# Kernel optimization log

Measured on AMD Instinct MI355X. Metric: run time of the kernel, lower is better.

## Reference

```python
import jax, jax.numpy as jnp
import numpy as np

N_NODES = 100000
N_EDGES = 1600000
IN_F = 32
HID = 128


def setup_inputs() -> dict:
    key = jax.random.key(0)
    ks = jax.random.split(key, 8)
    x = jax.random.normal(ks[0], (N_NODES, IN_F), dtype=jnp.float32)
    edge_index = jax.random.randint(ks[1], (2, N_EDGES), 0, N_NODES, dtype=jnp.int64)
    # Glorot-ish scaled weights
    W1 = jax.random.normal(ks[2], (IN_F, HID), dtype=jnp.float32) / np.sqrt(IN_F)
    b1 = jnp.zeros((HID,), dtype=jnp.float32)
    W2 = jax.random.normal(ks[3], (HID, HID), dtype=jnp.float32) / np.sqrt(HID)
    b2 = jnp.zeros((HID,), dtype=jnp.float32)
    W3 = jax.random.normal(ks[4], (HID, IN_F), dtype=jnp.float32) / np.sqrt(HID)
    b3 = jnp.zeros((IN_F,), dtype=jnp.float32)
    return {"x": x, "edge_index": edge_index, "W1": W1, "b1": b1,
            "W2": W2, "b2": b2, "W3": W3, "b3": b3}


def _gcn_norm(edge_index, n_nodes):
    # Add self-loops (PyG GCNConv default) and compute symmetric normalization
    loops = jnp.arange(n_nodes, dtype=edge_index.dtype)
    src = jnp.concatenate([edge_index[0], loops])
    dst = jnp.concatenate([edge_index[1], loops])
    ones = jnp.ones(src.shape[0], dtype=jnp.float32)
    deg = jax.ops.segment_sum(ones, dst, num_segments=n_nodes)
    deg_inv_sqrt = jnp.where(deg > 0, jax.lax.rsqrt(deg), 0.0)
    norm = deg_inv_sqrt[src] * deg_inv_sqrt[dst]  # [E + N]
    return src, dst, norm


def _gcn_conv(x, src, dst, norm, W, b, n_nodes):
    h = x @ W                                # [N, out] transform first (smaller msgs when out<in)
    msg = h[src] * norm[:, None]             # gather + edge-wise scale  [E+N, out]
    out = jax.ops.segment_sum(msg, dst, num_segments=n_nodes)  # scatter-add
    return out + b


def reference(x, edge_index, W1, b1, W2, b2, W3, b3):
    n = x.shape[0]
    src, dst, norm = _gcn_norm(edge_index, n)
    h = jax.nn.relu(_gcn_conv(x, src, dst, norm, W1, b1, n))
    h = jax.nn.relu(_gcn_conv(h, src, dst, norm, W2, b2, n))
    h = jax.nn.relu(_gcn_conv(h, src, dst, norm, W3, b3, n))
    return h
```

## Files before the change

kernel.cpp:

```cpp
#include <hip/hip_runtime.h>
#include <hip/hip_fp16.h>

#define N_NODES 100000
#define N_EDGES 1600000
#define IN_F 32
#define HID 128
#define BSHIFT 9
#define BSIZE 512
#define NBUCK 196
#define EPB 4096
#define NBB 391
#define REC_STRIDE 9728
#define COL_STRIDE 17408

typedef _Float16 half8 __attribute__((ext_vector_type(8)));
typedef float floatx4 __attribute__((ext_vector_type(4)));

__global__ __launch_bounds__(256) void k_wprep(const float* __restrict__ W1,
                                               const float* __restrict__ W2,
                                               const float* __restrict__ W3,
                                               _Float16* __restrict__ Wt) {
    const int bid = blockIdx.x, t = threadIdx.x;
    if (bid < 64) {
        int idx = bid * 256 + t;
        int n = idx >> 7, k = idx & 127;
        Wt[4096 + idx] = (_Float16)W2[k * HID + n];
    } else if (bid < 80) {
        int idx = (bid - 64) * 256 + t;
        int n = idx >> 5, k = idx & 31;
        Wt[n * 32 + k] = (_Float16)W1[k * HID + n];
    } else {
        int idx = (bid - 80) * 256 + t;
        int n = idx >> 7, k = idx & 127;
        Wt[20480 + idx] = (_Float16)W3[k * IN_F + n];
    }
}


__global__ __launch_bounds__(256) void k_bucket(const int* __restrict__ src,
                                                const int* __restrict__ dst,
                                                int* __restrict__ bcur,
                                                unsigned* __restrict__ rec) {
    __shared__ int hist[256];
    __shared__ int lbase[256];
    const int e0 = blockIdx.x * EPB;
    hist[threadIdx.x] = 0;
    __syncthreads();

    unsigned rk[16]; short bk[16];
#pragma unroll
    for (int k = 0; k < 16; ++k) {
        int e = e0 + k * 256 + threadIdx.x;
        if (e < N_EDGES) {
            int d = dst[e];
            int b = d >> BSHIFT;
            bk[k] = (short)b;
            rk[k] = ((unsigned)src[e] << BSHIFT) | (unsigned)(d & (BSIZE - 1));
            atomicAdd(&hist[b], 1);
        } else bk[k] = -1;
    }
    __syncthreads();
    int c = hist[threadIdx.x];
    lbase[threadIdx.x] =
        (c > 0) ? threadIdx.x * REC_STRIDE + atomicAdd(&bcur[threadIdx.x], c) : 0;
    __syncthreads();
    hist[threadIdx.x] = 0;
    __syncthreads();
#pragma unroll
    for (int k = 0; k < 16; ++k) {
        if (bk[k] >= 0) {
            int off = atomicAdd(&hist[bk[k]], 1);
            rec[lbase[bk[k]] + off] = rk[k];
        }
    }
}

__global__ __launch_bounds__(256) void k_fill3p(const unsigned* __restrict__ rec,
                                                const int* __restrict__ bcur,
                                                const float2* __restrict__ x2,
                                                int* __restrict__ ideg,
                                                int* __restrict__ cursor,
                                                int* __restrict__ col,
                                                __half2* __restrict__ t1) {
    __shared__ int lcnt[BSIZE];
    __shared__ int lcur[BSIZE];
    __shared__ int lend[BSIZE];
    __shared__ int s[256];
    const int b = blockIdx.x;
    const int t = threadIdx.x;
    const int n0 = b << BSHIFT;
    const int rbeg = b * REC_STRIDE;
    const int rend = rbeg + bcur[b];
    const int pbeg = b * COL_STRIDE;

    lcnt[t] = 0;
    lcnt[t + 256] = 0;
    __syncthreads();
    for (int i = rbeg + t; i < rend; i += 256)
        atomicAdd(&lcnt[rec[i] & (BSIZE - 1)], 1);
    __syncthreads();

    int a0 = lcnt[2 * t], a1 = lcnt[2 * t + 1];
    int p0 = (a0 + 15) & ~15, p1 = (a1 + 15) & ~15;
    int pv = p0 + p1;
    s[t] = pv;
    __syncthreads();
    for (int off = 1; off < 256; off <<= 1) {
        int v = (t >= off) ? s[t - off] : 0;
        __syncthreads();
        s[t] += v;
        __syncthreads();
    }
    int ex = s[t] - pv;
    int c0 = pbeg + ex;
    int c1 = c0 + p0;
    lcur[2 * t]     = c0;  lend[2 * t]     = c0 + p0;
    lcur[2 * t + 1] = c1;  lend[2 * t + 1] = c1 + p1;
    __syncthreads();

    for (int i = t; i < BSIZE; i += 256) {
        int n = n0 + i;
        if (n < N_NODES) {
            ideg[n]   = lcnt[i];
            cursor[n] = lcur[i];
        }
    }
    __syncthreads();
    for (int i = rbeg + t; i < rend; i += 256) {
        unsigned r = rec[i];
        int slot = atomicAdd(&lcur[r & (BSIZE - 1)], 1);
        col[slot] = (int)(r >> BSHIFT);
    }
    __syncthreads();
    for (int i = t; i < BSIZE; i += 256) {
        int e2 = lend[i];
        for (int k = lcur[i]; k < e2; ++k) col[k] = N_NODES;
    }

    if (b == 0 && t < 16) ((unsigned*)t1)[N_NODES * 16 + t] = 0u;
    for (int idx = t; idx < BSIZE * 16; idx += 256) {
        int loc = idx >> 4, j = idx & 15;
        int n = n0 + loc;
        if (n < N_NODES) {
            float dis = rsqrtf(1.0f + (float)lcnt[loc]);
            float2 v = x2[(size_t)n * 16 + j];
            t1[(size_t)n * 16 + j] = __floats2half2_rn(v.x * dis, v.y * dis);
        }
    }
}


__global__ __launch_bounds__(256) void k_gather32_pre(
    const int* __restrict__ cursor, const int* __restrict__ ideg,
    const int* __restrict__ col, const _Float16* __restrict__ T,
    _Float16* __restrict__ OUT) {
    const int lane = threadIdx.x & 63;
    const int slot = lane >> 2;
    const int fl   = lane & 3;
    const int wid  = blockIdx.x * 4 + (threadIdx.x >> 6);
    const int wstride = gridDim.x * 4;

    for (int node = wid; node < N_NODES; node += wstride) {
        int begin = cursor[node];
        int d     = ideg[node];
        int nb    = (d + 15) >> 4;
        float acc[8];
        if (slot == 0) {
            half8 v = *(const half8*)(T + (size_t)node * IN_F + fl * 8);
#pragma unroll
            for (int i = 0; i < 8; ++i) acc[i] = (float)v[i];
        } else {
#pragma unroll
            for (int i = 0; i < 8; ++i) acc[i] = 0.f;
        }
        const int* cp = col + begin + slot;
        int itb = 0;
        for (; itb + 2 <= nb; itb += 2, cp += 32) {
            int s0 = cp[0];
            int s1 = cp[16];
            half8 v0 = *(const half8*)(T + (size_t)s0 * IN_F + fl * 8);
            half8 v1 = *(const half8*)(T + (size_t)s1 * IN_F + fl * 8);
#pragma unroll
            for (int i = 0; i < 8; ++i) acc[i] += (float)v0[i] + (float)v1[i];
        }
        if (itb < nb) {
            int s0 = cp[0];
            half8 v0 = *(const half8*)(T + (size_t)s0 * IN_F + fl * 8);
#pragma unroll
            for (int i = 0; i < 8; ++i) acc[i] += (float)v0[i];
        }
#pragma unroll
        for (int m = 4; m < 64; m <<= 1)
#pragma unroll
            for (int i = 0; i < 8; ++i) acc[i] += __shfl_xor(acc[i], m, 64);
        if (slot == 0) {
            float dis = rsqrtf(1.0f + (float)d);
            half8 o;
#pragma unroll
            for (int i = 0; i < 8; ++i) o[i] = (_Float16)(acc[i] * dis);
            *(half8*)(OUT + (size_t)node * IN_F + fl * 8) = o;
        }
    }
}

__global__ __launch_bounds__(256) void k_gather32_fin(
    const int* __restrict__ cursor, const int* __restrict__ ideg,
    const int* __restrict__ col, const _Float16* __restrict__ T,
    const float* __restrict__ b, float* __restrict__ OUT) {
    const int lane = threadIdx.x & 63;
    const int slot = lane >> 2;
    const int fl   = lane & 3;
    const int wid  = blockIdx.x * 4 + (threadIdx.x >> 6);
    const int wstride = gridDim.x * 4;

    float4 bb0 = *(const float4*)(b + fl * 8);
    float4 bb1 = *(const float4*)(b + fl * 8 + 4);
    float bias[8] = {bb0.x, bb0.y, bb0.z, bb0.w, bb1.x, bb1.y, bb1.z, bb1.w};

    for (int node = wid; node < N_NODES; node += wstride) {
        int begin = cursor[node];
        int d     = ideg[node];
        int nb    = (d + 15) >> 4;
        float acc[8];
        if (slot == 0) {
            half8 v = *(const half8*)(T + (size_t)node * IN_F + fl * 8);
#pragma unroll
            for (int i = 0; i < 8; ++i) acc[i] = (float)v[i];
        } else {
#pragma unroll
            for (int i = 0; i < 8; ++i) acc[i] = 0.f;
        }
        const int* cp = col + begin + slot;
        int itb = 0;
        for (; itb + 2 <= nb; itb += 2, cp += 32) {
            int s0 = cp[0];
            int s1 = cp[16];
            half8 v0 = *(const half8*)(T + (size_t)s0 * IN_F + fl * 8);
            half8 v1 = *(const half8*)(T + (size_t)s1 * IN_F + fl * 8);
#pragma unroll
            for (int i = 0; i < 8; ++i) acc[i] += (float)v0[i] + (float)v1[i];
        }
        if (itb < nb) {
            int s0 = cp[0];
            half8 v0 = *(const half8*)(T + (size_t)s0 * IN_F + fl * 8);
#pragma unroll
            for (int i = 0; i < 8; ++i) acc[i] += (float)v0[i];
        }
#pragma unroll
        for (int m = 4; m < 64; m <<= 1)
#pragma unroll
            for (int i = 0; i < 8; ++i) acc[i] += __shfl_xor(acc[i], m, 64);
        if (slot == 0) {
            float dis = rsqrtf(1.0f + (float)d);
            float o[8];
#pragma unroll
            for (int i = 0; i < 8; ++i) {
                float v = acc[i] * dis + bias[i];
                o[i] = v > 0.f ? v : 0.f;
            }
            float* op = OUT + (size_t)node * IN_F + fl * 8;
            *(float4*)op       = make_float4(o[0], o[1], o[2], o[3]);
            *(float4*)(op + 4) = make_float4(o[4], o[5], o[6], o[7]);
        }
    }
}


__global__ __launch_bounds__(256, 4) void k_xform12(
    const _Float16* __restrict__ z, const _Float16* __restrict__ W1t,
    const float* __restrict__ b1, const _Float16* __restrict__ W2t,
    const int* __restrict__ ideg, _Float16* __restrict__ T) {
    if (blockIdx.x == 0 && threadIdx.x < 64)
        ((unsigned*)(T + (size_t)N_NODES * HID))[threadIdx.x] = 0u;
    __shared__ _Float16 H1s[64 * 136];

    const int lane = threadIdx.x & 63;
    const int wave = threadIdx.x >> 6;
    const int m16 = lane & 15, quad = lane >> 4;
    const int row0 = blockIdx.x * 64 + wave * 16;
    if (row0 >= N_NODES) return;

    {
        int arow = row0 + m16; if (arow >= N_NODES) arow = N_NODES - 1;
        half8 a = *(const half8*)(z + (size_t)arow * IN_F + quad * 8);
        floatx4 acc[8];
#pragma unroll
        for (int t = 0; t < 8; ++t) acc[t] = (floatx4){0.f, 0.f, 0.f, 0.f};
#pragma unroll
        for (int t = 0; t < 8; ++t) {
            half8 bf = *(const half8*)(W1t + (t * 16 + m16) * 32 + quad * 8);
            acc[t] = __builtin_amdgcn_mfma_f32_16x16x32_f16(a, bf, acc[t], 0, 0, 0);
        }
#pragma unroll
        for (int t = 0; t < 8; ++t) {
            int c = t * 16 + m16;
            float bj = b1[c];
#pragma unroll
            for (int r = 0; r < 4; ++r) {
                float v = acc[t][r] + bj;
                H1s[((wave * 16 + quad * 4 + r) * 136) + c] =
                    (_Float16)(v > 0.f ? v : 0.f);
            }
        }
    }
    __syncthreads();

    const _Float16* hp = &H1s[(wave * 16 + m16) * 136 + quad * 8];
    half8 a[4];
#pragma unroll
    for (int kk = 0; kk < 4; ++kk) a[kk] = *(const half8*)(hp + kk * 32);

    floatx4 acc[8];
#pragma unroll
    for (int t = 0; t < 8; ++t) acc[t] = (floatx4){0.f, 0.f, 0.f, 0.f};
#pragma unroll
    for (int t = 0; t < 8; ++t) {
        const _Float16* wp = W2t + (t * 16 + m16) * 128 + quad * 8;
#pragma unroll
        for (int kk = 0; kk < 4; ++kk) {
            half8 bf = *(const half8*)(wp + kk * 32);
            acc[t] = __builtin_amdgcn_mfma_f32_16x16x32_f16(a[kk], bf, acc[t], 0, 0, 0);
        }
    }
    float dis[4];
#pragma unroll
    for (int r = 0; r < 4; ++r) {
        int row = row0 + quad * 4 + r;
        dis[r] = (row < N_NODES) ? rsqrtf(1.0f + (float)ideg[row]) : 0.f;
    }
#pragma unroll
    for (int t = 0; t < 8; ++t) {
        int c = t * 16 + m16;
#pragma unroll
        for (int r = 0; r < 4; ++r) {
            int row = row0 + quad * 4 + r;
            if (row < N_NODES)
                T[(size_t)row * HID + c] = (_Float16)(acc[t][r] * dis[r]);
        }
    }
}

__global__ __launch_bounds__(256, 4) void k_g128x3(
    const int* __restrict__ cursor, const int* __restrict__ ideg,
    const int* __restrict__ col, const _Float16* __restrict__ T,
    const float* __restrict__ b2, const _Float16* __restrict__ W3t,
    _Float16* __restrict__ T3) {
    if (blockIdx.x == 0 && threadIdx.x < 16)
        ((unsigned*)(T3 + (size_t)N_NODES * IN_F))[threadIdx.x] = 0u;
    __shared__ _Float16 H2s[64 * 136];

    const int lane = threadIdx.x & 63;
    const int wave = threadIdx.x >> 6;
    const int slot = lane >> 4;
    const int fl   = lane & 15;
    const int row0 = blockIdx.x * 64;

    float4 bb0 = *(const float4*)(b2 + fl * 8);
    float4 bb1 = *(const float4*)(b2 + fl * 8 + 4);
    float bias[8] = {bb0.x, bb0.y, bb0.z, bb0.w, bb1.x, bb1.y, bb1.z, bb1.w};

    for (int k = 0; k < 16; ++k) {
        int node = row0 + wave * 16 + k;
        if (node >= N_NODES) break;
        int begin = cursor[node];
        int d     = ideg[node];
        int nb    = (d + 15) >> 4;
        float acc[8];
        if (slot == 0) {
            half8 v = *(const half8*)(T + (size_t)node * HID + fl * 8);
#pragma unroll
            for (int i = 0; i < 8; ++i) acc[i] = (float)v[i];
        } else {
#pragma unroll
            for (int i = 0; i < 8; ++i) acc[i] = 0.f;
        }
        const int* cp = col + begin + slot * 4;
        for (int itb = 0; itb < nb; ++itb, cp += 16) {
            int4 cc = *(const int4*)cp;
            half8 v0 = *(const half8*)(T + (size_t)cc.x * HID + fl * 8);
            half8 v1 = *(const half8*)(T + (size_t)cc.y * HID + fl * 8);
            half8 v2 = *(const half8*)(T + (size_t)cc.z * HID + fl * 8);
            half8 v3 = *(const half8*)(T + (size_t)cc.w * HID + fl * 8);
#pragma unroll
            for (int i = 0; i < 8; ++i)
                acc[i] += ((float)v0[i] + (float)v1[i]) + ((float)v2[i] + (float)v3[i]);
        }
#pragma unroll
        for (int m = 16; m < 64; m <<= 1)
#pragma unroll
            for (int i = 0; i < 8; ++i) acc[i] += __shfl_xor(acc[i], m, 64);
        if (slot == 0) {
            float dis = rsqrtf(1.0f + (float)d);
            half8 o;
#pragma unroll
            for (int i = 0; i < 8; ++i) {
                float v = acc[i] * dis + bias[i];
                o[i] = (_Float16)(v > 0.f ? v : 0.f);
            }
            *(half8*)&H2s[(wave * 16 + k) * 136 + fl * 8] = o;
        }
    }
    __syncthreads();

    const _Float16* hp = &H2s[(wave * 16 + fl) * 136 + slot * 8];
    half8 a[4];
#pragma unroll
    for (int kk = 0; kk < 4; ++kk) a[kk] = *(const half8*)(hp + kk * 32);

    floatx4 acc3[2];
#pragma unroll
    for (int t = 0; t < 2; ++t) acc3[t] = (floatx4){0.f, 0.f, 0.f, 0.f};
#pragma unroll
    for (int t = 0; t < 2; ++t) {
        const _Float16* wp = W3t + (t * 16 + fl) * 128 + slot * 8;
#pragma unroll
        for (int kk = 0; kk < 4; ++kk) {
            half8 bf = *(const half8*)(wp + kk * 32);
            acc3[t] = __builtin_amdgcn_mfma_f32_16x16x32_f16(a[kk], bf, acc3[t], 0, 0, 0);
        }
    }
    float dis[4];
#pragma unroll
    for (int r = 0; r < 4; ++r) {
        int row = row0 + wave * 16 + slot * 4 + r;
        dis[r] = (row < N_NODES) ? rsqrtf(1.0f + (float)ideg[row]) : 0.f;
    }
#pragma unroll
    for (int t = 0; t < 2; ++t) {
        int c = t * 16 + fl;
#pragma unroll
        for (int r = 0; r < 4; ++r) {
            int row = row0 + wave * 16 + slot * 4 + r;
            if (row < N_NODES)
                T3[(size_t)row * IN_F + c] = (_Float16)(acc3[t][r] * dis[r]);
        }
    }
}


extern "C" void kernel_launch(void* const* d_in, const int* in_sizes, int n_in,
                              void* d_out, int out_size, void* d_ws, size_t ws_size,
                              hipStream_t stream) {
    const float* x  = (const float*)d_in[0];
    const int*   ei = (const int*)d_in[1];
    const float* W1 = (const float*)d_in[2];
    const float* b1 = (const float*)d_in[3];
    const float* W2 = (const float*)d_in[4];
    const float* b2 = (const float*)d_in[5];
    const float* W3 = (const float*)d_in[6];
    const float* b3 = (const float*)d_in[7];
    float* out = (float*)d_out;

    const int* src = ei;
    const int* dst = ei + N_EDGES;

    int*      ideg   = (int*)d_ws;
    int*      cursor = ideg + 102400;
    int*      bcur   = cursor + 102400;
    int*      col    = bcur + 256;
    unsigned* rec    = (unsigned*)(col + NBUCK * COL_STRIDE);
    _Float16* Wt     = (_Float16*)(rec + NBUCK * REC_STRIDE);
    _Float16* t1h    = Wt + 24576;
    _Float16* z      = t1h + 3200064;
    _Float16* T2h    = z + 3200064;
    _Float16* T3h    = T2h + 12800128;

    const int xgrid = (N_NODES + 63) / 64;

    hipMemsetAsync(bcur, 0, 256 * sizeof(int), stream);
    k_wprep<<<96, 256, 0, stream>>>(W1, W2, W3, Wt);

    k_bucket<<<NBB, 256, 0, stream>>>(src, dst, bcur, rec);
    k_fill3p<<<NBUCK, 256, 0, stream>>>(rec, bcur, (const float2*)x,
                                        ideg, cursor, col, (__half2*)t1h);

    k_gather32_pre<<<2048, 256, 0, stream>>>(cursor, ideg, col, t1h, z);
    k_xform12<<<xgrid, 256, 0, stream>>>(z, Wt, b1, Wt + 4096, ideg, T2h);

    k_g128x3<<<xgrid, 256, 0, stream>>>(cursor, ideg, col, T2h, b2,
                                        Wt + 20480, T3h);

    k_gather32_fin<<<2048, 256, 0, stream>>>(cursor, ideg, col, T3h, b3, out);
}
```

Baseline: 323.9 us.

## Split 32-wide feature tables into two 16-wide planes for cache-friendlier gathers

The 32-feature fp16 node tables (t1, z, T3) are stored as two separate 16-column planes. The 32-wide gather kernels now make two passes, one per plane, with 32 edge slots per wave instead of 16. The idea is that each pass touches a table half the size, so more of it stays resident in L2/LLC during random neighbour gathers. Column padding per node grows to a multiple of 32 to match the wider slot count. The trade-offs are reading the column index lists twice, more padding work, and a larger col buffer; the 128-wide gather loop count is adjusted to the new padding.

```diff
diff --git a/kernel.cpp b/kernel.cpp
--- a/kernel.cpp
+++ b/kernel.cpp
@@ -11,7 +11,8 @@
 #define EPB 4096
 #define NBB 391
 #define REC_STRIDE 9728
-#define COL_STRIDE 17408
+#define COL_STRIDE 25600
+#define ZSL 1600016
 
 typedef _Float16 half8 __attribute__((ext_vector_type(8)));
 typedef float floatx4 __attribute__((ext_vector_type(4)));
@@ -81,7 +82,7 @@
                                                 int* __restrict__ ideg,
                                                 int* __restrict__ cursor,
                                                 int* __restrict__ col,
-                                                __half2* __restrict__ t1) {
+                                                _Float16* __restrict__ t1) {
     __shared__ int lcnt[BSIZE];
     __shared__ int lcur[BSIZE];
     __shared__ int lend[BSIZE];
@@ -101,7 +102,7 @@
     __syncthreads();
 
     int a0 = lcnt[2 * t], a1 = lcnt[2 * t + 1];
-    int p0 = (a0 + 15) & ~15, p1 = (a1 + 15) & ~15;
+    int p0 = (a0 + 31) & ~31, p1 = (a1 + 31) & ~31;
     int pv = p0 + p1;
     s[t] = pv;
     __syncthreads();
@@ -137,14 +138,19 @@
         for (int k = lcur[i]; k < e2; ++k) col[k] = N_NODES;
     }
 
-    if (b == 0 && t < 16) ((unsigned*)t1)[N_NODES * 16 + t] = 0u;
+    if (b == 0 && t < 16) {
+        if (t < 8) ((unsigned*)(t1 + (size_t)N_NODES * 16))[t] = 0u;
+        else       ((unsigned*)(t1 + ZSL + (size_t)N_NODES * 16))[t - 8] = 0u;
+    }
     for (int idx = t; idx < BSIZE * 16; idx += 256) {
         int loc = idx >> 4, j = idx & 15;
         int n = n0 + loc;
         if (n < N_NODES) {
             float dis = rsqrtf(1.0f + (float)lcnt[loc]);
             float2 v = x2[(size_t)n * 16 + j];
-            t1[(size_t)n * 16 + j] = __floats2half2_rn(v.x * dis, v.y * dis);
+            int p = j >> 3, jj = j & 7;
+            *(__half2*)(t1 + (size_t)p * ZSL + (size_t)n * 16 + jj * 2) =
+                __floats2half2_rn(v.x * dis, v.y * dis);
         }
     }
 }
@@ -155,50 +161,54 @@
     const int* __restrict__ col, const _Float16* __restrict__ T,
     _Float16* __restrict__ OUT) {
     const int lane = threadIdx.x & 63;
-    const int slot = lane >> 2;
-    const int fl   = lane & 3;
+    const int slot = lane >> 1;
+    const int fl   = lane & 1;
     const int wid  = blockIdx.x * 4 + (threadIdx.x >> 6);
     const int wstride = gridDim.x * 4;
 
-    for (int node = wid; node < N_NODES; node += wstride) {
-        int begin = cursor[node];
-        int d     = ideg[node];
-        int nb    = (d + 15) >> 4;
-        float acc[8];
-        if (slot == 0) {
-            half8 v = *(const half8*)(T + (size_t)node * IN_F + fl * 8);
-#pragma unroll
-            for (int i = 0; i < 8; ++i) acc[i] = (float)v[i];
-        } else {
-#pragma unroll
-            for (int i = 0; i < 8; ++i) acc[i] = 0.f;
-        }
-        const int* cp = col + begin + slot;
-        int itb = 0;
-        for (; itb + 2 <= nb; itb += 2, cp += 32) {
-            int s0 = cp[0];
-            int s1 = cp[16];
-            half8 v0 = *(const half8*)(T + (size_t)s0 * IN_F + fl * 8);
-            half8 v1 = *(const half8*)(T + (size_t)s1 * IN_F + fl * 8);
-#pragma unroll
-            for (int i = 0; i < 8; ++i) acc[i] += (float)v0[i] + (float)v1[i];
-        }
-        if (itb < nb) {
-            int s0 = cp[0];
-            half8 v0 = *(const half8*)(T + (size_t)s0 * IN_F + fl * 8);
-#pragma unroll
-            for (int i = 0; i < 8; ++i) acc[i] += (float)v0[i];
-        }
-#pragma unroll
-        for (int m = 4; m < 64; m <<= 1)
-#pragma unroll
-            for (int i = 0; i < 8; ++i) acc[i] += __shfl_xor(acc[i], m, 64);
-        if (slot == 0) {
-            float dis = rsqrtf(1.0f + (float)d);
-            half8 o;
-#pragma unroll
-            for (int i = 0; i < 8; ++i) o[i] = (_Float16)(acc[i] * dis);
-            *(half8*)(OUT + (size_t)node * IN_F + fl * 8) = o;
+    for (int p = 0; p < 2; ++p) {
+        const _Float16* Tp = T + (size_t)p * ZSL;
+        _Float16* Op = OUT + (size_t)p * ZSL;
+        for (int node = wid; node < N_NODES; node += wstride) {
+            int begin = cursor[node];
+            int d     = ideg[node];
+            int nb    = (d + 31) >> 5;
+            float acc[8];
+            if (slot == 0) {
+                half8 v = *(const half8*)(Tp + (size_t)node * 16 + fl * 8);
+#pragma unroll
+                for (int i = 0; i < 8; ++i) acc[i] = (float)v[i];
+            } else {
+#pragma unroll
+                for (int i = 0; i < 8; ++i) acc[i] = 0.f;
+            }
+            const int* cp = col + begin + slot;
+            int itb = 0;
+            for (; itb + 2 <= nb; itb += 2, cp += 64) {
+                int s0 = cp[0];
+                int s1 = cp[32];
+                half8 v0 = *(const half8*)(Tp + (size_t)s0 * 16 + fl * 8);
+                half8 v1 = *(const half8*)(Tp + (size_t)s1 * 16 + fl * 8);
+#pragma unroll
+                for (int i = 0; i < 8; ++i) acc[i] += (float)v0[i] + (float)v1[i];
+            }
+            if (itb < nb) {
+                int s0 = cp[0];
+                half8 v0 = *(const half8*)(Tp + (size_t)s0 * 16 + fl * 8);
+#pragma unroll
+                for (int i = 0; i < 8; ++i) acc[i] += (float)v0[i];
+            }
+#pragma unroll
+            for (int m = 2; m < 64; m <<= 1)
+#pragma unroll
+                for (int i = 0; i < 8; ++i) acc[i] += __shfl_xor(acc[i], m, 64);
+            if (slot == 0) {
+                float dis = rsqrtf(1.0f + (float)d);
+                half8 o;
+#pragma unroll
+                for (int i = 0; i < 8; ++i) o[i] = (_Float16)(acc[i] * dis);
+                *(half8*)(Op + (size_t)node * 16 + fl * 8) = o;
+            }
         }
     }
 }
@@ -208,59 +218,61 @@
     const int* __restrict__ col, const _Float16* __restrict__ T,
     const float* __restrict__ b, float* __restrict__ OUT) {
     const int lane = threadIdx.x & 63;
-    const int slot = lane >> 2;
-    const int fl   = lane & 3;
+    const int slot = lane >> 1;
+    const int fl   = lane & 1;
     const int wid  = blockIdx.x * 4 + (threadIdx.x >> 6);
     const int wstride = gridDim.x * 4;
 
-    float4 bb0 = *(const float4*)(b + fl * 8);
-    float4 bb1 = *(const float4*)(b + fl * 8 + 4);
-    float bias[8] = {bb0.x, bb0.y, bb0.z, bb0.w, bb1.x, bb1.y, bb1.z, bb1.w};
-
-    for (int node = wid; node < N_NODES; node += wstride) {
-        int begin = cursor[node];
-        int d     = ideg[node];
-        int nb    = (d + 15) >> 4;
-        float acc[8];
-        if (slot == 0) {
-            half8 v = *(const half8*)(T + (size_t)node * IN_F + fl * 8);
-#pragma unroll
-            for (int i = 0; i < 8; ++i) acc[i] = (float)v[i];
-        } else {
-#pragma unroll
-            for (int i = 0; i < 8; ++i) acc[i] = 0.f;
-        }
-        const int* cp = col + begin + slot;
-        int itb = 0;
-        for (; itb + 2 <= nb; itb += 2, cp += 32) {
-            int s0 = cp[0];
-            int s1 = cp[16];
-            half8 v0 = *(const half8*)(T + (size_t)s0 * IN_F + fl * 8);
-            half8 v1 = *(const half8*)(T + (size_t)s1 * IN_F + fl * 8);
-#pragma unroll
-            for (int i = 0; i < 8; ++i) acc[i] += (float)v0[i] + (float)v1[i];
-        }
-        if (itb < nb) {
-            int s0 = cp[0];
-            half8 v0 = *(const half8*)(T + (size_t)s0 * IN_F + fl * 8);
-#pragma unroll
-            for (int i = 0; i < 8; ++i) acc[i] += (float)v0[i];
-        }
-#pragma unroll
-        for (int m = 4; m < 64; m <<= 1)
-#pragma unroll
-            for (int i = 0; i < 8; ++i) acc[i] += __shfl_xor(acc[i], m, 64);
-        if (slot == 0) {
-            float dis = rsqrtf(1.0f + (float)d);
-            float o[8];
-#pragma unroll
-            for (int i = 0; i < 8; ++i) {
-                float v = acc[i] * dis + bias[i];
-                o[i] = v > 0.f ? v : 0.f;
-            }
-            float* op = OUT + (size_t)node * IN_F + fl * 8;
-            *(float4*)op       = make_float4(o[0], o[1], o[2], o[3]);
-            *(float4*)(op + 4) = make_float4(o[4], o[5], o[6], o[7]);
+    for (int p = 0; p < 2; ++p) {
+        const _Float16* Tp = T + (size_t)p * ZSL;
+        float4 bb0 = *(const float4*)(b + p * 16 + fl * 8);
+        float4 bb1 = *(const float4*)(b + p * 16 + fl * 8 + 4);
+        float bias[8] = {bb0.x, bb0.y, bb0.z, bb0.w, bb1.x, bb1.y, bb1.z, bb1.w};
+        for (int node = wid; node < N_NODES; node += wstride) {
+            int begin = cursor[node];
+            int d     = ideg[node];
+            int nb    = (d + 31) >> 5;
+            float acc[8];
+            if (slot == 0) {
+                half8 v = *(const half8*)(Tp + (size_t)node * 16 + fl * 8);
+#pragma unroll
+                for (int i = 0; i < 8; ++i) acc[i] = (float)v[i];
+            } else {
+#pragma unroll
+                for (int i = 0; i < 8; ++i) acc[i] = 0.f;
+            }
+            const int* cp = col + begin + slot;
+            int itb = 0;
+            for (; itb + 2 <= nb; itb += 2, cp += 64) {
+                int s0 = cp[0];
+                int s1 = cp[32];
+                half8 v0 = *(const half8*)(Tp + (size_t)s0 * 16 + fl * 8);
+                half8 v1 = *(const half8*)(Tp + (size_t)s1 * 16 + fl * 8);
+#pragma unroll
+                for (int i = 0; i < 8; ++i) acc[i] += (float)v0[i] + (float)v1[i];
+            }
+            if (itb < nb) {
+                int s0 = cp[0];
+                half8 v0 = *(const half8*)(Tp + (size_t)s0 * 16 + fl * 8);
+#pragma unroll
+                for (int i = 0; i < 8; ++i) acc[i] += (float)v0[i];
+            }
+#pragma unroll
+            for (int m = 2; m < 64; m <<= 1)
+#pragma unroll
+                for (int i = 0; i < 8; ++i) acc[i] += __shfl_xor(acc[i], m, 64);
+            if (slot == 0) {
+                float dis = rsqrtf(1.0f + (float)d);
+                float o[8];
+#pragma unroll
+                for (int i = 0; i < 8; ++i) {
+                    float v = acc[i] * dis + bias[i];
+                    o[i] = v > 0.f ? v : 0.f;
+                }
+                float* op = OUT + (size_t)node * IN_F + p * 16 + fl * 8;
+                *(float4*)op       = make_float4(o[0], o[1], o[2], o[3]);
+                *(float4*)(op + 4) = make_float4(o[4], o[5], o[6], o[7]);
+            }
         }
     }
 }
@@ -282,7 +294,8 @@
 
     {
         int arow = row0 + m16; if (arow >= N_NODES) arow = N_NODES - 1;
-        half8 a = *(const half8*)(z + (size_t)arow * IN_F + quad * 8);
+        half8 a = *(const half8*)(z + (size_t)(quad >> 1) * ZSL +
+                                  (size_t)arow * 16 + (quad & 1) * 8);
         floatx4 acc[8];
 #pragma unroll
         for (int t = 0; t < 8; ++t) acc[t] = (floatx4){0.f, 0.f, 0.f, 0.f};
@@ -345,8 +358,11 @@
     const int* __restrict__ col, const _Float16* __restrict__ T,
     const float* __restrict__ b2, const _Float16* __restrict__ W3t,
     _Float16* __restrict__ T3) {
-    if (blockIdx.x == 0 && threadIdx.x < 16)
-        ((unsigned*)(T3 + (size_t)N_NODES * IN_F))[threadIdx.x] = 0u;
+    if (blockIdx.x == 0 && threadIdx.x < 16) {
+        int t = threadIdx.x;
+        if (t < 8) ((unsigned*)(T3 + (size_t)N_NODES * 16))[t] = 0u;
+        else       ((unsigned*)(T3 + ZSL + (size_t)N_NODES * 16))[t - 8] = 0u;
+    }
     __shared__ _Float16 H2s[64 * 136];
 
     const int lane = threadIdx.x & 63;
@@ -364,7 +380,7 @@
         if (node >= N_NODES) break;
         int begin = cursor[node];
         int d     = ideg[node];
-        int nb    = (d + 15) >> 4;
+        int nb    = ((d + 31) & ~31) >> 4;
         float acc[8];
         if (slot == 0) {
             half8 v = *(const half8*)(T + (size_t)node * HID + fl * 8);
@@ -427,12 +443,12 @@
     }
 #pragma unroll
     for (int t = 0; t < 2; ++t) {
-        int c = t * 16 + fl;
 #pragma unroll
         for (int r = 0; r < 4; ++r) {
             int row = row0 + wave * 16 + slot * 4 + r;
             if (row < N_NODES)
-                T3[(size_t)row * IN_F + c] = (_Float16)(acc3[t][r] * dis[r]);
+                T3[(size_t)t * ZSL + (size_t)row * 16 + fl] =
+                    (_Float16)(acc3[t][r] * dis[r]);
         }
     }
 }
@@ -461,8 +477,8 @@
     unsigned* rec    = (unsigned*)(col + NBUCK * COL_STRIDE);
     _Float16* Wt     = (_Float16*)(rec + NBUCK * REC_STRIDE);
     _Float16* t1h    = Wt + 24576;
-    _Float16* z      = t1h + 3200064;
-    _Float16* T2h    = z + 3200064;
+    _Float16* z      = t1h + 2 * ZSL + 16;
+    _Float16* T2h    = z + 2 * ZSL + 16;
     _Float16* T3h    = T2h + 12800128;
 
     const int xgrid = (N_NODES + 63) / 64;
@@ -472,7 +488,7 @@
 
     k_bucket<<<NBB, 256, 0, stream>>>(src, dst, bcur, rec);
     k_fill3p<<<NBUCK, 256, 0, stream>>>(rec, bcur, (const float2*)x,
-                                        ideg, cursor, col, (__half2*)t1h);
+                                        ideg, cursor, col, t1h);
 
     k_gather32_pre<<<2048, 256, 0, stream>>>(cursor, ideg, col, t1h, z);
     k_xform12<<<xgrid, 256, 0, stream>>>(z, Wt, b1, Wt + 4096, ideg, T2h);
```

After: 461.7 us. 42.6% more time.
